# Kernel tuning notes

Measured on AMD Instinct MI355X. Metric: run time of the kernel, lower is better.

Reference implementation:

```python
import jax, jax.numpy as jnp
import numpy as np

# --- config (matches init_kwargs) ---
HID = 2048      # hidden_size
H = 16          # num_attention_heads
D_NOPE = 128    # qk_nope_head_dim
D_ROPE = 64     # qk_rope_head_dim
D_Q = D_NOPE + D_ROPE  # 192
D_V = 128       # v_head_dim
QR = 1536       # q_lora_rank
KVR = 512       # kv_lora_rank
PH = 16         # pattern_heads
PD = HID // PH  # 128
THETA = 10000.0
EPS = 1e-6


def rmsnorm(x, w):
    var = jnp.mean(jnp.square(x), axis=-1, keepdims=True)
    return x * jax.lax.rsqrt(var + EPS) * w


def rope_cos_sin(seq_len):
    inv_freq = 1.0 / (THETA ** (jnp.arange(0, D_ROPE, 2, dtype=jnp.float32) / D_ROPE))
    t = jnp.arange(seq_len, dtype=jnp.float32)
    freqs = jnp.outer(t, inv_freq)            # [S, D_ROPE/2]
    emb = jnp.concatenate([freqs, freqs], -1)  # [S, D_ROPE]
    return jnp.cos(emb), jnp.sin(emb)


def rotate_half(x):
    x1, x2 = jnp.split(x, 2, axis=-1)
    return jnp.concatenate([-x2, x1], axis=-1)


def apply_rope(x, cos, sin):
    # x: [B, H, S, D_ROPE]; cos/sin: [S, D_ROPE]
    return x * cos[None, None] + rotate_half(x) * sin[None, None]


def setup_inputs() -> dict:
    key = jax.random.key(0)
    ks = jax.random.split(key, 12)
    def w(k, shape):
        return (jax.random.normal(k, shape, jnp.float32) / np.sqrt(shape[-1])).astype(jnp.float32)
    B, S = 2, 1024
    return {
        "hidden_states": jax.random.normal(ks[0], (B, S, HID), jnp.float32),
        "q_a_w": w(ks[1], (QR, HID)),
        "q_a_ln_w": jnp.ones((QR,), jnp.float32),
        "q_b_w": w(ks[2], (H * D_Q, QR)),
        "kv_a_w": w(ks[3], (KVR + H * D_ROPE, HID)),
        "kv_a_ln_w": jnp.ones((KVR,), jnp.float32),
        "kv_b_w": w(ks[4], (H * (D_NOPE + D_V), KVR)),
        "o_w": w(ks[5], (HID, H * D_V)),
        "sp_q_w": w(ks[6], (HID, HID)),
        "sp_k_w": w(ks[7], (HID, HID)),
        "sp_v_w": w(ks[8], (HID, HID)),
        "sp_o_w": w(ks[9], (HID, HID)),
        "gate_w": w(ks[10], (2, HID)),
        "gate_b": jnp.zeros((2,), jnp.float32),
    }


def reference(hidden_states, q_a_w, q_a_ln_w, q_b_w, kv_a_w, kv_a_ln_w, kv_b_w,
              o_w, sp_q_w, sp_k_w, sp_v_w, sp_o_w, gate_w, gate_b):
    b, s, _ = hidden_states.shape
    dt = hidden_states.dtype

    # ---- main MLA path ----
    q_mid = rmsnorm(hidden_states @ q_a_w.T, q_a_ln_w)                      # [B,S,QR]
    q = (q_mid @ q_b_w.T).reshape(b, s, H, D_Q).transpose(0, 2, 1, 3)       # [B,H,S,Dq]
    q_nope, q_pe = q[..., :D_NOPE], q[..., D_NOPE:]

    kv_a = hidden_states @ kv_a_w.T                                         # [B,S,KVR+H*Dr]
    kv_lora, k_pe_flat = kv_a[..., :KVR], kv_a[..., KVR:]
    k_pe = k_pe_flat.reshape(b, s, H, D_ROPE).transpose(0, 2, 1, 3)         # [B,H,S,Dr]

    kv = (rmsnorm(kv_lora, kv_a_ln_w) @ kv_b_w.T)
    kv = kv.reshape(b, s, H, D_NOPE + D_V).transpose(0, 2, 1, 3)            # [B,H,S,Dn+Dv]
    k_nope, v = kv[..., :D_NOPE], kv[..., D_NOPE:]

    cos, sin = rope_cos_sin(s)
    q_pe = apply_rope(q_pe, cos, sin)
    k_pe = apply_rope(k_pe, cos, sin)

    qf = jnp.concatenate([q_nope, q_pe], -1)                                # [B,H,S,Dq]
    kf = jnp.concatenate([k_nope, k_pe], -1)

    scale = D_Q ** -0.5
    scores = jnp.einsum('bhqd,bhkd->bhqk', qf, kf) * scale
    probs = jax.nn.softmax(scores.astype(jnp.float32), axis=-1).astype(dt)
    ctx = jnp.einsum('bhqk,bhkd->bhqd', probs, v)                           # [B,H,S,Dv]
    main_out = ctx.transpose(0, 2, 1, 3).reshape(b, s, H * D_V) @ o_w.T     # [B,S,HID]

    # ---- self pattern path (standard MHA on hidden_states) ----
    def split_heads(x):
        return x.reshape(b, s, PH, PD).transpose(0, 2, 1, 3)
    pq = split_heads(hidden_states @ sp_q_w.T)
    pk = split_heads(hidden_states @ sp_k_w.T)
    pv = split_heads(hidden_states @ sp_v_w.T)
    p_scores = jnp.einsum('bhqd,bhkd->bhqk', pq, pk) * (PD ** -0.5)
    p_probs = jax.nn.softmax(p_scores.astype(jnp.float32), axis=-1).astype(dt)
    p_ctx = jnp.einsum('bhqk,bhkd->bhqd', p_probs, pv)
    pattern_out = p_ctx.transpose(0, 2, 1, 3).reshape(b, s, HID) @ sp_o_w.T

    # ---- learned gate over paths ----
    gates = jax.nn.softmax(hidden_states @ gate_w.T + gate_b, axis=-1)      # [B,S,2]
    return gates[..., 0:1] * main_out + gates[..., 1:2] * pattern_out
```

## Files before the change

### kernel.cpp

```cpp
#include <hip/hip_runtime.h>
#include <math.h>
#include <stdint.h>

#define HIDN  2048
#define NH    16
#define DNOPE 128
#define DROPE 64
#define DQ    192
#define DV    128
#define QRANK 1536
#define KVRANK 512
#define SEQ   1024
#define NBATCH 2
#define NTOK  (NBATCH*SEQ)
#define EPSV  1e-6f

typedef unsigned short u16;
typedef unsigned int   u32;
typedef __attribute__((ext_vector_type(8))) short  short8;
typedef __attribute__((ext_vector_type(8))) unsigned short ushort8;
typedef __attribute__((ext_vector_type(4))) float  f32x4;

__device__ __forceinline__ u16 f2b(float f) {
    u32 u = __float_as_uint(f);
    u = (u + 0x7fffu + ((u >> 16) & 1u)) >> 16;
    return (u16)u;
}
__device__ __forceinline__ float b2f(u16 h) {
    return __uint_as_float(((u32)h) << 16);
}

__device__ __forceinline__ void async_copy16(const u16* g, u16* l) {
    __builtin_amdgcn_global_load_lds(
        (const __attribute__((address_space(1))) u32*)g,
        (__attribute__((address_space(3))) u32*)l,
        16, 0, 0);
}

__device__ __forceinline__ int swz(int r, int c) { return r * 4 + (c ^ ((r >> 1) & 3)); }

#define DPP_ROR(x, ctrl) __int_as_float(__builtin_amdgcn_update_dpp( \
    __float_as_int(x), __float_as_int(x), ctrl, 0xF, 0xF, false))

__device__ __forceinline__ float rowmax16(float x) {
    x = fmaxf(x, DPP_ROR(x, 0x121));
    x = fmaxf(x, DPP_ROR(x, 0x122));
    x = fmaxf(x, DPP_ROR(x, 0x124));
    x = fmaxf(x, DPP_ROR(x, 0x128));
    return x;
}
__device__ __forceinline__ float rowsum16(float x) {
    x += DPP_ROR(x, 0x121);
    x += DPP_ROR(x, 0x122);
    x += DPP_ROR(x, 0x124);
    x += DPP_ROR(x, 0x128);
    return x;
}

struct CastArgs {
    const float* s[10];
    u16* d[10];
    int cum[11];
    const float* lnq;
    const float* lnkv;
};
__global__ __launch_bounds__(256)
void cast_all(CastArgs a, int total_chunks)
{
    int c = blockIdx.x * 256 + threadIdx.x;
    if (c >= total_chunks) return;
    int seg = 0;
    #pragma unroll
    for (int i = 1; i < 10; ++i) seg += (c >= a.cum[i]) ? 1 : 0;
    int local = c - a.cum[seg];
    const float* src = a.s[seg] + (size_t)local * 8;
    u16* dst = a.d[seg] + (size_t)local * 8;
    float4 x = *(const float4*)(src);
    float4 y = *(const float4*)(src + 4);
    if (seg == 3 || seg == 4) {
        const float* ln = (seg == 3) ? a.lnq : a.lnkv;
        u32 kmod = (seg == 3) ? (u32)QRANK : (u32)KVRANK;
        u32 kb = ((u32)local * 8u) % kmod;
        float4 w0 = *(const float4*)(ln + kb);
        float4 w1 = *(const float4*)(ln + kb + 4);
        x.x *= w0.x; x.y *= w0.y; x.z *= w0.z; x.w *= w0.w;
        y.x *= w1.x; y.y *= w1.y; y.z *= w1.z; y.w *= w1.w;
    }
    ushort8 o;
    o[0]=f2b(x.x); o[1]=f2b(x.y); o[2]=f2b(x.z); o[3]=f2b(x.w);
    o[4]=f2b(y.x); o[5]=f2b(y.y); o[6]=f2b(y.z); o[7]=f2b(y.w);
    *(ushort8*)(dst) = o;
}

struct GemmSeg {
    const u16* X; const u16* W;
    float* Cf; u16* Cb; u16* Cb2; u16* Cb3;
    int K; int ldx; int ldc; int mode; int bx0;
};
struct GemmArgs { GemmSeg seg[3]; int nseg; float* ssq; float* sskv; };

__global__ __launch_bounds__(256)
void gemm_multi(GemmArgs a)
{
    __shared__ __align__(16) u16 As[2 * 4096];
    __shared__ __align__(16) u16 Bs[2 * 4096];
    int s = 0;
    if (a.nseg > 1 && (int)blockIdx.y >= a.seg[1].bx0) s = 1;
    if (a.nseg > 2 && (int)blockIdx.y >= a.seg[2].bx0) s = 2;
    const GemmSeg g = a.seg[s];

    const int tid = threadIdx.x;
    const int bn = ((int)blockIdx.y - g.bx0) * 128;
    const int bm = blockIdx.x * 128;
    const int lane = tid & 63, wv = tid >> 6;
    const int lm = lane & 15, lq = lane >> 4;
    const int wm = (wv >> 1) * 64, wn = (wv & 1) * 64;
    const int ldx = g.ldx, K = g.K;
    const u16* Xp = g.X;
    const u16* Wp = g.W;

    auto stage = [&](int kt, int buf) {
        int k0 = kt * 32;
        #pragma unroll
        for (int it = 0; it < 2; ++it) {
            int base = wv * 64 + it * 256;
            int slot = base + lane;
            int r = slot >> 2, c = (slot & 3) ^ ((r >> 1) & 3);
            async_copy16(Xp + (size_t)(bm + r) * ldx + k0 + c * 8,
                         As + buf * 4096 + base * 8);
            async_copy16(Wp + (size_t)(bn + r) * K + k0 + c * 8,
                         Bs + buf * 4096 + base * 8);
        }
    };

    f32x4 acc[4][4] = {};
    const int niter = K >> 5;
    stage(0, 0);
    for (int kt = 0; kt < niter; ++kt) {
        int cur = kt & 1;
        __syncthreads();
        if (kt + 1 < niter) stage(kt + 1, cur ^ 1);
        const u16* Ab = As + cur * 4096;
        const u16* Bb = Bs + cur * 4096;
        short8 af[4], bf[4];
        #pragma unroll
        for (int mt = 0; mt < 4; ++mt) {
            int R = wm + mt * 16 + lm;
            af[mt] = *(const short8*)(Ab + swz(R, lq) * 8);
        }
        #pragma unroll
        for (int nt = 0; nt < 4; ++nt) {
            int R = wn + nt * 16 + lm;
            bf[nt] = *(const short8*)(Bb + swz(R, lq) * 8);
        }
        #pragma unroll
        for (int mt = 0; mt < 4; ++mt)
            #pragma unroll
            for (int nt = 0; nt < 4; ++nt)
                acc[mt][nt] = __builtin_amdgcn_mfma_f32_16x16x32_bf16(
                    af[mt], bf[nt], acc[mt][nt], 0, 0, 0);
    }

    const int mode = g.mode;
    if (mode == 1) {
        const int h2  = (bn + wn) / DQ;
        const int hd0 = (bn + wn) % DQ;
        const bool ropeH = (hd0 == 128);
        float invf0 = 0.f, invf1 = 0.f;
        if (ropeH) {
            invf0 = exp2f((float)lm * -0.41524101186f);
            invf1 = exp2f((float)(16 + lm) * -0.41524101186f);
        }
        #pragma unroll
        for (int mt = 0; mt < 4; ++mt) {
            int token0 = bm + wm + mt * 16 + lq * 4;
            #pragma unroll
            for (int i = 0; i < 4; ++i) {
                int tok = token0 + i;
                int b2 = tok >> 10, s2 = tok & (SEQ - 1);
                float inv = rsqrtf(a.ssq[tok] * (1.f / QRANK) + EPSV);
                u16* row = g.Cb + ((size_t)((b2 * NH + h2) * SEQ + s2)) * DQ + hd0;
                if (!ropeH) {
                    #pragma unroll
                    for (int nt = 0; nt < 4; ++nt)
                        row[nt * 16 + lm] = f2b(acc[mt][nt][i] * inv);
                } else {
                    float sn0, c0, sn1, c1;
                    sincosf((float)s2 * invf0, &sn0, &c0);
                    sincosf((float)s2 * invf1, &sn1, &c1);
                    float x10 = acc[mt][0][i] * inv, x20 = acc[mt][2][i] * inv;
                    float x11 = acc[mt][1][i] * inv, x21 = acc[mt][3][i] * inv;
                    row[lm]          = f2b(x10 * c0 - x20 * sn0);
                    row[32 + lm]     = f2b(x20 * c0 + x10 * sn0);
                    row[16 + lm]     = f2b(x11 * c1 - x21 * sn1);
                    row[48 + lm]     = f2b(x21 * c1 + x11 * sn1);
                }
            }
        }
        return;
    }
    #pragma unroll
    for (int mt = 0; mt < 4; ++mt) {
        int token0 = bm + wm + mt * 16 + lq * 4;
        #pragma unroll
        for (int i = 0; i < 4; ++i) {
            int tok = token0 + i;
            int b2 = tok >> 10, s2 = tok & (SEQ - 1);
            float invkv = 1.f;
            if (mode == 3) invkv = rsqrtf(a.sskv[tok] * (1.f / KVRANK) + EPSV);
            #pragma unroll
            for (int nt = 0; nt < 4; ++nt) {
                int feat = bn + wn + nt * 16 + lm;
                float v = acc[mt][nt][i];
                if (mode == 0) {
                    g.Cf[(size_t)tok * g.ldc + feat] = v;
                } else if (mode == 5) {
                    g.Cb[(size_t)tok * g.ldc + feat] = f2b(v);
                } else if (mode == 3) {
                    v *= invkv;
                    int h2 = feat >> 8, c = feat & 255;
                    if (c < 128)
                        g.Cb[((size_t)((b2 * NH + h2) * SEQ + s2)) * DQ + c] = f2b(v);
                    else
                        g.Cb2[((size_t)((b2 * NH + h2) * 128 + (c - 128))) * SEQ + s2] = f2b(v);
                } else {
                    int wsel = feat >> 11;
                    int f2 = feat & 2047;
                    int h2 = f2 >> 7, d = f2 & 127;
                    if (wsel == 0)
                        g.Cb[((size_t)((b2 * NH + h2) * SEQ + s2)) * 128 + d] = f2b(v);
                    else if (wsel == 1)
                        g.Cb2[((size_t)((b2 * NH + h2) * SEQ + s2)) * 128 + d] = f2b(v);
                    else
                        g.Cb3[((size_t)((b2 * NH + h2) * 128 + d)) * SEQ + s2] = f2b(v);
                }
            }
        }
    }
    if (mode == 5) {
        float* ssp = nullptr;
        if (bn < QRANK) ssp = a.ssq;
        else if (bn < QRANK + KVRANK) ssp = a.sskv;
        if (ssp) {
            #pragma unroll
            for (int mt = 0; mt < 4; ++mt) {
                int token0 = bm + wm + mt * 16 + lq * 4;
                #pragma unroll
                for (int i = 0; i < 4; ++i) {
                    float sq = 0.f;
                    #pragma unroll
                    for (int nt = 0; nt < 4; ++nt) {
                        float v = acc[mt][nt][i];
                        sq += v * v;
                    }
                    sq = rowsum16(sq);
                    if (lm == 0) atomicAdd(&ssp[token0 + i], sq);
                }
            }
        }
    }
}

__global__ __launch_bounds__(256)
void gemm_oproj(const u16* __restrict__ ctxp, const u16* __restrict__ ow,
                const u16* __restrict__ pctxp, const u16* __restrict__ spw,
                const float2* __restrict__ gates, float* __restrict__ out)
{
    __shared__ __align__(16) u16 As[2 * 4096];
    __shared__ __align__(16) u16 Bs[2 * 4096];
    const int tid = threadIdx.x;
    const int bn = blockIdx.y * 128;
    const int bm = blockIdx.x * 128;
    const int lane = tid & 63, wv = tid >> 6;
    const int lm = lane & 15, lq = lane >> 4;
    const int wm = (wv >> 1) * 64, wn = (wv & 1) * 64;

    f32x4 acc0[4][4] = {};
    f32x4 acc1[4][4] = {};

    auto kloop = [&](const u16* Xp, const u16* Wp, f32x4 (&acc)[4][4]) {
        auto stage = [&](int kt, int buf) {
            int k0 = kt * 32;
            #pragma unroll
            for (int it = 0; it < 2; ++it) {
                int base = wv * 64 + it * 256;
                int slot = base + lane;
                int r = slot >> 2, c = (slot & 3) ^ ((r >> 1) & 3);
                async_copy16(Xp + (size_t)(bm + r) * HIDN + k0 + c * 8,
                             As + buf * 4096 + base * 8);
                async_copy16(Wp + (size_t)(bn + r) * HIDN + k0 + c * 8,
                             Bs + buf * 4096 + base * 8);
            }
        };
        const int niter = HIDN >> 5;
        stage(0, 0);
        for (int kt = 0; kt < niter; ++kt) {
            int cur = kt & 1;
            __syncthreads();
            if (kt + 1 < niter) stage(kt + 1, cur ^ 1);
            const u16* Ab = As + cur * 4096;
            const u16* Bb = Bs + cur * 4096;
            short8 af[4], bf[4];
            #pragma unroll
            for (int mt = 0; mt < 4; ++mt)
                af[mt] = *(const short8*)(Ab + swz(wm + mt * 16 + lm, lq) * 8);
            #pragma unroll
            for (int nt = 0; nt < 4; ++nt)
                bf[nt] = *(const short8*)(Bb + swz(wn + nt * 16 + lm, lq) * 8);
            #pragma unroll
            for (int mt = 0; mt < 4; ++mt)
                #pragma unroll
                for (int nt = 0; nt < 4; ++nt)
                    acc[mt][nt] = __builtin_amdgcn_mfma_f32_16x16x32_bf16(
                        af[mt], bf[nt], acc[mt][nt], 0, 0, 0);
        }
    };

    kloop(ctxp,  ow,  acc0);
    kloop(pctxp, spw, acc1);

    #pragma unroll
    for (int mt = 0; mt < 4; ++mt) {
        int token0 = bm + wm + mt * 16 + lq * 4;
        #pragma unroll
        for (int i = 0; i < 4; ++i) {
            int tok = token0 + i;
            float2 gv = gates[tok];
            float* orow = out + (size_t)tok * HIDN;
            #pragma unroll
            for (int nt = 0; nt < 4; ++nt) {
                int feat = bn + wn + nt * 16 + lm;
                orow[feat] = gv.x * acc0[mt][nt][i] + gv.y * acc1[mt][nt][i];
            }
        }
    }
}

__global__ __launch_bounds__(256)
void gate_kern(const float* __restrict__ x, const float* __restrict__ gw,
               const float* __restrict__ gb, float2* __restrict__ gates)
{
    const int tok = blockIdx.x;
    const float* xr = x + (size_t)tok * HIDN;
    float d0 = 0.f, d1 = 0.f;
    for (int i = threadIdx.x; i < HIDN; i += 256) {
        float v = xr[i];
        d0 += v * gw[i];
        d1 += v * gw[HIDN + i];
    }
    __shared__ float r0[256], r1[256];
    r0[threadIdx.x] = d0; r1[threadIdx.x] = d1;
    __syncthreads();
    for (int off = 128; off > 0; off >>= 1) {
        if (threadIdx.x < off) {
            r0[threadIdx.x] += r0[threadIdx.x + off];
            r1[threadIdx.x] += r1[threadIdx.x + off];
        }
        __syncthreads();
    }
    if (threadIdx.x == 0) {
        float l0 = r0[0] + gb[0], l1 = r1[0] + gb[1];
        float m = fmaxf(l0, l1);
        float e0 = __expf(l0 - m), e1 = __expf(l1 - m);
        float inv = 1.f / (e0 + e1);
        gates[tok] = make_float2(e0 * inv, e1 * inv);
    }
}

__global__ __launch_bounds__(256)
void rope_k(const u16* __restrict__ amid, u16* __restrict__ kf)
{
    int t = blockIdx.x * 256 + threadIdx.x;
    int i = t & 31, s = (t >> 5) & (SEQ - 1), bh = t >> 15;
    float inv_freq = exp2f((float)i * -0.41524101186f);
    float ang = (float)s * inv_freq;
    float c, sn; sincosf(ang, &sn, &c);
    int h = bh & (NH - 1), bb = bh >> 4;
    const u16* src = amid + ((size_t)(bb * SEQ + s)) * 3072 + (QRANK + KVRANK) + h * DROPE;
    float x1 = b2f(src[i]), x2 = b2f(src[32 + i]);
    u16* dst = kf + ((size_t)bh * SEQ + s) * DQ + DNOPE;
    dst[i]      = f2b(x1 * c - x2 * sn);
    dst[32 + i] = f2b(x2 * c + x1 * sn);
}

template<int DQK>
__device__ __forceinline__
void flash_body(const u16* __restrict__ Q, const u16* __restrict__ Kf,
                const u16* __restrict__ Vt, u16* __restrict__ ctx_out,
                float scale, u16* Ks, u16* Vs, u16* Ps, int qt, int h, int bb)
{
    constexpr int KSZ  = 32 * DQK;
    constexpr int VSZ  = 32 * 128;
    constexpr int NKIT = DQK / 64;
    constexpr int NT   = SEQ / 32;
    const int tid = threadIdx.x, lane = tid & 63, wv = tid >> 6;
    const int lm = lane & 15, lq = lane >> 4;
    const size_t bh = (size_t)bb * NH + h;
    const u16* Qb = Q + (bh * SEQ + qt * 128 + wv * 32) * (size_t)DQK;
    const u16* Kb = Kf + bh * SEQ * (size_t)DQK;
    const u16* Vb = Vt + bh * (size_t)128 * SEQ;

    short8 qfrag[2][DQK / 32];
    #pragma unroll
    for (int rh = 0; rh < 2; ++rh)
        #pragma unroll
        for (int ks = 0; ks < DQK / 32; ++ks)
            qfrag[rh][ks] = *(const short8*)(Qb + (rh * 16 + lm) * DQK + ks * 32 + lq * 8);

    auto stage = [&](int kt, int buf) {
        #pragma unroll
        for (int it = 0; it < NKIT; ++it) {
            int base = it * 256 + wv * 64;
            int slot = base + lane;
            int plane = slot >> 7, rem = slot & 127;
            int key = rem >> 2, c = (rem & 3) ^ ((key >> 1) & 3);
            async_copy16(Kb + (size_t)(kt * 32 + key) * DQK + plane * 32 + c * 8,
                         Ks + buf * KSZ + base * 8);
        }
        #pragma unroll
        for (int it = 0; it < 2; ++it) {
            int base = it * 256 + wv * 64;
            int slot = base + lane;
            int d = slot >> 2, c = (slot & 3) ^ ((d >> 1) & 3);
            async_copy16(Vb + (size_t)d * SEQ + kt * 32 + c * 8,
                         Vs + buf * VSZ + base * 8);
        }
    };

    float m_i[2][4], l_i[2][4];
    #pragma unroll
    for (int rh = 0; rh < 2; ++rh)
        #pragma unroll
        for (int i = 0; i < 4; ++i) { m_i[rh][i] = -INFINITY; l_i[rh][i] = 0.f; }
    f32x4 oacc[2][8] = {};

    stage(0, 0);
    for (int kt = 0; kt < NT; ++kt) {
        int cur = kt & 1;
        __syncthreads();
        if (kt + 1 < NT) stage(kt + 1, cur ^ 1);
        const u16* Kc = Ks + cur * KSZ;
        const u16* Vc = Vs + cur * VSZ;

        f32x4 sacc[2][2] = {};
        #pragma unroll
        for (int kb = 0; kb < 2; ++kb)
            #pragma unroll
            for (int ks = 0; ks < DQK / 32; ++ks) {
                int R = kb * 16 + lm;
                short8 kfr = *(const short8*)(Kc + ks * 1024 + swz(R, lq) * 8);
                sacc[0][kb] = __builtin_amdgcn_mfma_f32_16x16x32_bf16(
                    qfrag[0][ks], kfr, sacc[0][kb], 0, 0, 0);
                sacc[1][kb] = __builtin_amdgcn_mfma_f32_16x16x32_bf16(
                    qfrag[1][ks], kfr, sacc[1][kb], 0, 0, 0);
            }

        float p0[2][4], p1[2][4], mx[2][4];
        bool needb = false;
        #pragma unroll
        for (int rh = 0; rh < 2; ++rh)
            #pragma unroll
            for (int i = 0; i < 4; ++i) {
                float s0 = sacc[rh][0][i] * scale, s1 = sacc[rh][1][i] * scale;
                float m2 = rowmax16(fmaxf(s0, s1));
                p0[rh][i] = s0; p1[rh][i] = s1; mx[rh][i] = m2;
                needb |= (m2 > m_i[rh][i] + 8.f);
            }
        bool need = __any(needb);
        float alpha[2][4];
        if (need) {
            #pragma unroll
            for (int rh = 0; rh < 2; ++rh)
                #pragma unroll
                for (int i = 0; i < 4; ++i) {
                    float mnew = fmaxf(m_i[rh][i], mx[rh][i]);
                    alpha[rh][i] = __expf(m_i[rh][i] - mnew);
                    m_i[rh][i] = mnew;
                    l_i[rh][i] *= alpha[rh][i];
                }
        }
        #pragma unroll
        for (int rh = 0; rh < 2; ++rh)
            #pragma unroll
            for (int i = 0; i < 4; ++i) {
                p0[rh][i] = __expf(p0[rh][i] - m_i[rh][i]);
                p1[rh][i] = __expf(p1[rh][i] - m_i[rh][i]);
                l_i[rh][i] += rowsum16(p0[rh][i] + p1[rh][i]);
            }

        u16* Pw = Ps + wv * 1280;
        #pragma unroll
        for (int rh = 0; rh < 2; ++rh)
            #pragma unroll
            for (int i = 0; i < 4; ++i) {
                Pw[(rh * 16 + lq * 4 + i) * 40 + lm]      = f2b(p0[rh][i]);
                Pw[(rh * 16 + lq * 4 + i) * 40 + 16 + lm] = f2b(p1[rh][i]);
            }
        short8 pfrag0 = *(const short8*)(Pw + lm * 40 + lq * 8);
        short8 pfrag1 = *(const short8*)(Pw + (16 + lm) * 40 + lq * 8);

        if (need) {
            #pragma unroll
            for (int rh = 0; rh < 2; ++rh)
                #pragma unroll
                for (int nt = 0; nt < 8; ++nt)
                    #pragma unroll
                    for (int i = 0; i < 4; ++i) oacc[rh][nt][i] *= alpha[rh][i];
        }
        #pragma unroll
        for (int nt = 0; nt < 8; ++nt) {
            int R = nt * 16 + lm;
            short8 vfr = *(const short8*)(Vc + swz(R, lq) * 8);
            oacc[0][nt] = __builtin_amdgcn_mfma_f32_16x16x32_bf16(
                pfrag0, vfr, oacc[0][nt], 0, 0, 0);
            oacc[1][nt] = __builtin_amdgcn_mfma_f32_16x16x32_bf16(
                pfrag1, vfr, oacc[1][nt], 0, 0, 0);
        }
    }

    #pragma unroll
    for (int rh = 0; rh < 2; ++rh) {
        int s0 = qt * 128 + wv * 32 + rh * 16 + lq * 4;
        #pragma unroll
        for (int i = 0; i < 4; ++i) {
            float inv = 1.f / l_i[rh][i];
            u16* dst = ctx_out + ((size_t)(bb * SEQ + s0 + i) * NH + h) * 128;
            #pragma unroll
            for (int nt = 0; nt < 8; ++nt)
                dst[nt * 16 + lm] = f2b(oacc[rh][nt][i] * inv);
        }
    }
}

__global__ __launch_bounds__(256, 2)
void flash_fused(const u16* qf, const u16* kf, const u16* Vtg, u16* ctx,
                 const u16* pq, const u16* pk, const u16* pvt, u16* p_ctx,
                 float scale_main, float scale_pat)
{
    __shared__ __align__(16) u16 Ks[2 * 32 * DQ];
    __shared__ __align__(16) u16 Vs[2 * 32 * 128];
    __shared__ __align__(16) u16 Ps[4 * 32 * 40];
    int h = blockIdx.x, qtb = blockIdx.y, bb = blockIdx.z;
    if (qtb < 8)
        flash_body<DQ>(qf, kf, Vtg, ctx, scale_main, Ks, Vs, Ps, qtb, h, bb);
    else
        flash_body<128>(pq, pk, pvt, p_ctx, scale_pat, Ks, Vs, Ps, qtb - 8, h, bb);
}

extern "C" void kernel_launch(void* const* d_in, const int* in_sizes, int n_in,
                              void* d_out, int out_size, void* d_ws, size_t ws_size,
                              hipStream_t stream)
{
    const float* X        = (const float*)d_in[0];
    const float* q_a_w    = (const float*)d_in[1];
    const float* q_a_ln_w = (const float*)d_in[2];
    const float* q_b_w    = (const float*)d_in[3];
    const float* kv_a_w   = (const float*)d_in[4];
    const float* kv_a_ln_w= (const float*)d_in[5];
    const float* kv_b_w   = (const float*)d_in[6];
    const float* o_w      = (const float*)d_in[7];
    const float* sp_q_w   = (const float*)d_in[8];
    const float* sp_k_w   = (const float*)d_in[9];
    const float* sp_v_w   = (const float*)d_in[10];
    const float* sp_o_w   = (const float*)d_in[11];
    const float* gate_w   = (const float*)d_in[12];
    const float* gate_b   = (const float*)d_in[13];
    float* out = (float*)d_out;

    char* p = (char*)d_ws;
    auto alloc = [&](size_t bytes) -> char* {
        char* r = p; p += (bytes + 255) & ~(size_t)255; return r;
    };
    u16* amid      = (u16*)alloc((size_t)NTOK * 3072 * 2);
    u16* Xb        = (u16*)alloc((size_t)NTOK * HIDN * 2);
    u16* aw_b      = (u16*)alloc((size_t)3072 * HIDN * 2);
    u16* q_b_wb    = (u16*)alloc((size_t)NH * DQ * QRANK * 2);
    u16* kv_b_wb   = (u16*)alloc((size_t)NH * 256 * KVRANK * 2);
    u16* o_wb      = (u16*)alloc((size_t)HIDN * HIDN * 2);
    u16* spqkv_wb  = (u16*)alloc((size_t)3 * HIDN * HIDN * 2);
    u16* sp_o_wb   = (u16*)alloc((size_t)HIDN * HIDN * 2);
    u16* qf        = (u16*)alloc((size_t)NTOK * NH * DQ * 2);
    u16* kf        = (u16*)alloc((size_t)NTOK * NH * DQ * 2);
    u16* Vtg       = (u16*)alloc((size_t)NBATCH * NH * 128 * SEQ * 2);
    u16* pq        = (u16*)alloc((size_t)NTOK * HIDN * 2);
    u16* pk        = (u16*)alloc((size_t)NTOK * HIDN * 2);
    float* ssbuf   = (float*)alloc((size_t)2 * NTOK * 4);
    float2* gates  = (float2*)alloc((size_t)NTOK * 8);
    u16* pvt    = aw_b;
    u16* ctx    = q_b_wb;
    u16* p_ctx  = spqkv_wb;
    float* ss_q  = ssbuf;
    float* ss_kv = ssbuf + NTOK;

    dim3 blk(256);

    hipMemsetAsync(ssbuf, 0, (size_t)2 * NTOK * 4, stream);

    CastArgs ca;
    const float* srcs[10] = {X, q_a_w, kv_a_w, q_b_w, kv_b_w, o_w,
                             sp_q_w, sp_k_w, sp_v_w, sp_o_w};
    u16* dsts[10] = {Xb, aw_b, aw_b + (size_t)QRANK * HIDN, q_b_wb, kv_b_wb, o_wb,
                     spqkv_wb, spqkv_wb + (size_t)HIDN * HIDN,
                     spqkv_wb + (size_t)2 * HIDN * HIDN, sp_o_wb};
    int ns[10] = {NTOK * HIDN, QRANK * HIDN, 1536 * HIDN, NH * DQ * QRANK,
                  NH * 256 * KVRANK, HIDN * HIDN, HIDN * HIDN, HIDN * HIDN,
                  HIDN * HIDN, HIDN * HIDN};
    int cum = 0;
    for (int i = 0; i < 10; ++i) {
        ca.s[i] = srcs[i]; ca.d[i] = dsts[i];
        ca.cum[i] = cum; cum += ns[i] / 8;
    }
    ca.cum[10] = cum;
    ca.lnq = q_a_ln_w; ca.lnkv = kv_a_ln_w;
    cast_all<<<dim3((cum + 255) / 256), blk, 0, stream>>>(ca, cum);

    gate_kern<<<dim3(NTOK), blk, 0, stream>>>(X, gate_w, gate_b, gates);

    {
        GemmArgs ga = {};
        ga.nseg = 1;
        ga.seg[0] = {Xb, aw_b, nullptr, amid, nullptr, nullptr,
                     HIDN, HIDN, 3072, 5, 0};
        ga.ssq = ss_q; ga.sskv = ss_kv;
        gemm_multi<<<dim3(16, 24), blk, 0, stream>>>(ga);
    }

    {
        GemmArgs ga = {};
        ga.nseg = 3;
        ga.seg[0] = {Xb, spqkv_wb, nullptr, pq, pk, pvt,
                     HIDN, HIDN, 0, 4, 0};
        ga.seg[1] = {amid, q_b_wb, nullptr, qf, nullptr, nullptr,
                     QRANK, 3072, 0, 1, 48};
        ga.seg[2] = {amid + QRANK, kv_b_wb, nullptr, kf, Vtg, nullptr,
                     KVRANK, 3072, 0, 3, 72};
        ga.ssq = ss_q; ga.sskv = ss_kv;
        gemm_multi<<<dim3(16, 104), blk, 0, stream>>>(ga);
    }

    rope_k<<<dim3(4096), blk, 0, stream>>>(amid, kf);

    flash_fused<<<dim3(NH, 16, NBATCH), blk, 0, stream>>>(
        qf, kf, Vtg, ctx, pq, pk, pvt, p_ctx,
        1.0f / sqrtf((float)DQ), 1.0f / sqrtf(128.0f));

    gemm_oproj<<<dim3(16, 16), blk, 0, stream>>>(
        ctx, o_wb, p_ctx, sp_o_wb, gates, out);
}
```

Measured before the change: 557.8 us.

## Split output projection K-loops across two 256-thread groups in one block

```diff
diff --git a/kernel.cpp b/kernel.cpp
--- a/kernel.cpp
+++ b/kernel.cpp
@@ -261,76 +261,93 @@
     }
 }
 
-__global__ __launch_bounds__(256)
+__global__ __launch_bounds__(512)
 void gemm_oproj(const u16* __restrict__ ctxp, const u16* __restrict__ ow,
                 const u16* __restrict__ pctxp, const u16* __restrict__ spw,
                 const float2* __restrict__ gates, float* __restrict__ out)
 {
-    __shared__ __align__(16) u16 As[2 * 4096];
-    __shared__ __align__(16) u16 Bs[2 * 4096];
+    __shared__ __align__(16) u16 As[2][2 * 4096];
+    __shared__ __align__(16) u16 Bs[2][2 * 4096];
     const int tid = threadIdx.x;
+    const int grp = tid >> 8;
+    const int gtid = tid & 255;
+    const int lane = gtid & 63, wv = gtid >> 6;
+    const int lm = lane & 15, lq = lane >> 4;
+    const int wm = (wv >> 1) * 64, wn = (wv & 1) * 64;
     const int bn = blockIdx.y * 128;
     const int bm = blockIdx.x * 128;
-    const int lane = tid & 63, wv = tid >> 6;
-    const int lm = lane & 15, lq = lane >> 4;
-    const int wm = (wv >> 1) * 64, wn = (wv & 1) * 64;
-
-    f32x4 acc0[4][4] = {};
-    f32x4 acc1[4][4] = {};
-
-    auto kloop = [&](const u16* Xp, const u16* Wp, f32x4 (&acc)[4][4]) {
-        auto stage = [&](int kt, int buf) {
-            int k0 = kt * 32;
-            #pragma unroll
-            for (int it = 0; it < 2; ++it) {
-                int base = wv * 64 + it * 256;
-                int slot = base + lane;
-                int r = slot >> 2, c = (slot & 3) ^ ((r >> 1) & 3);
-                async_copy16(Xp + (size_t)(bm + r) * HIDN + k0 + c * 8,
-                             As + buf * 4096 + base * 8);
-                async_copy16(Wp + (size_t)(bn + r) * HIDN + k0 + c * 8,
-                             Bs + buf * 4096 + base * 8);
-            }
-        };
-        const int niter = HIDN >> 5;
-        stage(0, 0);
-        for (int kt = 0; kt < niter; ++kt) {
-            int cur = kt & 1;
-            __syncthreads();
-            if (kt + 1 < niter) stage(kt + 1, cur ^ 1);
-            const u16* Ab = As + cur * 4096;
-            const u16* Bb = Bs + cur * 4096;
-            short8 af[4], bf[4];
-            #pragma unroll
-            for (int mt = 0; mt < 4; ++mt)
-                af[mt] = *(const short8*)(Ab + swz(wm + mt * 16 + lm, lq) * 8);
+
+    const u16* Xp = grp ? pctxp : ctxp;
+    const u16* Wp = grp ? spw   : ow;
+    u16* Ag = As[grp];
+    u16* Bg = Bs[grp];
+
+    auto stage = [&](int kt, int buf) {
+        int k0 = kt * 32;
+        #pragma unroll
+        for (int it = 0; it < 2; ++it) {
+            int base = wv * 64 + it * 256;
+            int slot = base + lane;
+            int r = slot >> 2, c = (slot & 3) ^ ((r >> 1) & 3);
+            async_copy16(Xp + (size_t)(bm + r) * HIDN + k0 + c * 8,
+                         Ag + buf * 4096 + base * 8);
+            async_copy16(Wp + (size_t)(bn + r) * HIDN + k0 + c * 8,
+                         Bg + buf * 4096 + base * 8);
+        }
+    };
+
+    f32x4 acc[4][4] = {};
+    const int niter = HIDN >> 5;
+    stage(0, 0);
+    for (int kt = 0; kt < niter; ++kt) {
+        int cur = kt & 1;
+        __syncthreads();
+        if (kt + 1 < niter) stage(kt + 1, cur ^ 1);
+        const u16* Ab = Ag + cur * 4096;
+        const u16* Bb = Bg + cur * 4096;
+        short8 af[4], bf[4];
+        #pragma unroll
+        for (int mt = 0; mt < 4; ++mt)
+            af[mt] = *(const short8*)(Ab + swz(wm + mt * 16 + lm, lq) * 8);
+        #pragma unroll
+        for (int nt = 0; nt < 4; ++nt)
+            bf[nt] = *(const short8*)(Bb + swz(wn + nt * 16 + lm, lq) * 8);
+        #pragma unroll
+        for (int mt = 0; mt < 4; ++mt)
             #pragma unroll
             for (int nt = 0; nt < 4; ++nt)
-                bf[nt] = *(const short8*)(Bb + swz(wn + nt * 16 + lm, lq) * 8);
-            #pragma unroll
-            for (int mt = 0; mt < 4; ++mt)
+                acc[mt][nt] = __builtin_amdgcn_mfma_f32_16x16x32_bf16(
+                    af[mt], bf[nt], acc[mt][nt], 0, 0, 0);
+    }
+
+    float* cb = (float*)&As[0][0];
+    #pragma unroll
+    for (int mt = 0; mt < 4; ++mt) {
+        __syncthreads();
+        if (grp == 1) {
+            #pragma unroll
+            for (int i = 0; i < 4; ++i) {
+                int tok = bm + wm + mt * 16 + lq * 4 + i;
+                float g1 = gates[tok].y;
+                int rr = (wv >> 1) * 16 + lq * 4 + i;
                 #pragma unroll
                 for (int nt = 0; nt < 4; ++nt)
-                    acc[mt][nt] = __builtin_amdgcn_mfma_f32_16x16x32_bf16(
-                        af[mt], bf[nt], acc[mt][nt], 0, 0, 0);
-        }
-    };
-
-    kloop(ctxp,  ow,  acc0);
-    kloop(pctxp, spw, acc1);
-
-    #pragma unroll
-    for (int mt = 0; mt < 4; ++mt) {
-        int token0 = bm + wm + mt * 16 + lq * 4;
-        #pragma unroll
-        for (int i = 0; i < 4; ++i) {
-            int tok = token0 + i;
-            float2 gv = gates[tok];
-            float* orow = out + (size_t)tok * HIDN;
-            #pragma unroll
-            for (int nt = 0; nt < 4; ++nt) {
-                int feat = bn + wn + nt * 16 + lm;
-                orow[feat] = gv.x * acc0[mt][nt][i] + gv.y * acc1[mt][nt][i];
+                    cb[rr * 132 + wn + nt * 16 + lm] = g1 * acc[mt][nt][i];
+            }
+        }
+        __syncthreads();
+        if (grp == 0) {
+            #pragma unroll
+            for (int i = 0; i < 4; ++i) {
+                int tok = bm + wm + mt * 16 + lq * 4 + i;
+                float g0 = gates[tok].x;
+                int rr = (wv >> 1) * 16 + lq * 4 + i;
+                float* orow = out + (size_t)tok * HIDN;
+                #pragma unroll
+                for (int nt = 0; nt < 4; ++nt) {
+                    int col = wn + nt * 16 + lm;
+                    orow[bn + col] = g0 * acc[mt][nt][i] + cb[rr * 132 + col];
+                }
             }
         }
     }
@@ -644,6 +661,6 @@
         qf, kf, Vtg, ctx, pq, pk, pvt, p_ctx,
         1.0f / sqrtf((float)DQ), 1.0f / sqrtf(128.0f));
 
-    gemm_oproj<<<dim3(16, 16), blk, 0, stream>>>(
+    gemm_oproj<<<dim3(16, 16), dim3(512), 0, stream>>>(
         ctx, o_wb, p_ctx, sp_o_wb, gates, out);
 }
```

Result: no change. 548.7 us (-1.6%).
